# Kernel optimization log

Measured on AMD Instinct MI355X. Metric: run time of the kernel, lower is better.

## Reference

```python
import jax, jax.numpy as jnp
import numpy as np

B, S, D_ENC, D_DEC, UNITS = 32, 2048, 1024, 1024, 1024


def setup_inputs() -> dict:
    key = jax.random.key(0)
    k1, k2, k3, k4 = jax.random.split(key, 4)
    h_encoder = jax.random.normal(k1, (B, S, D_ENC), dtype=jnp.float32)
    h_decoder_prev = jax.random.normal(k2, (B, D_DEC), dtype=jnp.float32)
    # Dense1: (D_ENC + D_DEC) -> UNITS, tanh; Dense2: UNITS -> 1, relu
    W1 = jax.random.normal(k3, (D_ENC + D_DEC, UNITS), dtype=jnp.float32) * 0.02
    b1 = jnp.zeros((UNITS,), dtype=jnp.float32)
    W2 = jax.random.normal(k4, (UNITS, 1), dtype=jnp.float32) * 0.02
    b2 = jnp.zeros((1,), dtype=jnp.float32)
    return {"h_encoder": h_encoder, "h_decoder_prev": h_decoder_prev,
            "W1": W1, "b1": b1, "W2": W2, "b2": b2}


def reference(h_encoder, h_decoder_prev, W1, b1, W2, b2):
    # Equivalent to concat([h_encoder, repeat(h_decoder)], -1) @ W1 without
    # materializing the repeated/concatenated tensor: split W1 by input block.
    d_enc = h_encoder.shape[-1]
    W1_enc, W1_dec = W1[:d_enc], W1[d_enc:]
    dec_proj = h_decoder_prev @ W1_dec  # [B, UNITS]
    energies1 = jnp.tanh(jnp.einsum('bse,eu->bsu', h_encoder, W1_enc)
                         + dec_proj[:, None, :] + b1)  # [B, S, UNITS]
    energies2 = jax.nn.relu(jnp.einsum('bsu,uo->bso', energies1, W2) + b2)  # [B, S, 1]
    attention_weights = jax.nn.softmax(energies2, axis=1)  # softmax over seq axis
    # repeat along last dim + multiply + reduce_sum == broadcast-weighted sum
    context_vector = jnp.sum(attention_weights * h_encoder, axis=1)  # [B, D_ENC]
    return (context_vector, attention_weights)
```

## Files before the change

kernel.cpp:

```cpp
#include <hip/hip_runtime.h>
#include <cstdint>
#include <cstddef>

#define BB 32
#define SS 2048
#define DD 1024
#define MM (BB * SS)

typedef __bf16 bf16_t;
typedef __bf16 bf16x4 __attribute__((ext_vector_type(4)));
typedef __bf16 bf16x8 __attribute__((ext_vector_type(8)));
typedef float  f32x4  __attribute__((ext_vector_type(4)));

typedef __attribute__((address_space(1))) unsigned int gu32;
typedef __attribute__((address_space(3))) unsigned int lu32;

__device__ __forceinline__ void async_copy16(const void* g, void* l) {
  __builtin_amdgcn_global_load_lds((gu32*)g, (lu32*)l, 16, 0, 0);
}

__global__ __launch_bounds__(256) void convert_henc_kernel(
    const float* __restrict__ h, bf16_t* __restrict__ o) {
  const size_t base = ((size_t)blockIdx.x * 256 + threadIdx.x) * 8;
#pragma unroll
  for (int it = 0; it < 16; ++it) {
    const size_t off = base + (size_t)it * 4194304;
    const float4 a = *(const float4*)(h + off);
    const float4 b = *(const float4*)(h + off + 4);
    bf16x8 r;
    r[0] = (bf16_t)a.x; r[1] = (bf16_t)a.y; r[2] = (bf16_t)a.z; r[3] = (bf16_t)a.w;
    r[4] = (bf16_t)b.x; r[5] = (bf16_t)b.y; r[6] = (bf16_t)b.z; r[7] = (bf16_t)b.w;
    *(bf16x8*)(o + off) = r;
  }
}

__global__ __launch_bounds__(256) void conv_w1t_kernel(
    const float* __restrict__ W1, bf16_t* __restrict__ W1T) {
  __shared__ float tile[64][65];
  const int bk = (blockIdx.x & 15) * 64;
  const int bn = (blockIdx.x >> 4) * 64;
  const int tx = threadIdx.x & 63;
  const int ty = threadIdx.x >> 6;
#pragma unroll
  for (int i = 0; i < 16; ++i) {
    const int kr = i * 4 + ty;
    tile[kr][tx] = W1[(size_t)(bk + kr) * 1024 + bn + tx];
  }
  __syncthreads();
#pragma unroll
  for (int i = 0; i < 16; ++i) {
    const int nr = i * 4 + ty;
    W1T[(size_t)(bn + nr) * 1024 + bk + tx] = (bf16_t)tile[tx][nr];
  }
}

__global__ __launch_bounds__(256) void dec_proj_kernel(
    const float* __restrict__ hDec, const float* __restrict__ W1,
    const float* __restrict__ b1, float* __restrict__ dp,
    float* __restrict__ e2) {
  __shared__ float sred[256];
  const int bidx = blockIdx.x;
  const int b  = bidx >> 3;
  const int uc = bidx & 7;
  const int t  = threadIdx.x;
  if (e2) e2[bidx * 256 + t] = 0.f;
  const int u  = uc * 128 + (t & 127);
  const int kh = t >> 7;
  const float* wd = W1 + (size_t)1024 * 1024 + u;
  const float* hd = hDec + b * 1024 + kh * 512;
  float acc = 0.f;
#pragma unroll 4
  for (int k = 0; k < 512; ++k)
    acc += hd[k] * wd[(size_t)(kh * 512 + k) * 1024];
  sred[t] = acc;
  __syncthreads();
  if (t < 128) dp[b * 1024 + u] = sred[t] + sred[t + 128] + b1[u];
}

__global__ __launch_bounds__(256, 3) void fused_gemm_v2(
    const bf16_t* __restrict__ hEncB, const bf16_t* __restrict__ W1T,
    const float* __restrict__ dp, const float* __restrict__ W2,
    float* __restrict__ e2p) {
  __shared__ bf16_t sA[2 * 128 * 32];
  __shared__ bf16_t sB[2 * 128 * 32];

  const int tid  = threadIdx.x;
  const int lane = tid & 63;
  const int wv   = tid >> 6;
  const int wm   = wv >> 1;
  const int wn   = wv & 1;

  const int bid   = blockIdx.x;
  const int mtile = ((bid >> 6) << 3) | (bid & 7);
  const int nblk  = (bid >> 3) & 7;
  const int m0    = mtile * 128;
  const int n0    = nblk * 128;
  const int b     = m0 >> 11;

  const int col = lane & 15;
  const int q   = lane >> 4;
  const int sw  = q ^ ((col >> 1) & 3);

  f32x4 acc[4][4];
#pragma unroll
  for (int mi = 0; mi < 4; ++mi)
#pragma unroll
    for (int ni = 0; ni < 4; ++ni)
      acc[mi][ni] = (f32x4){0.f, 0.f, 0.f, 0.f};

  char* sAc = (char*)sA;
  char* sBc = (char*)sB;

  const int lrow = lane >> 2;
  const int lc   = (lane & 3) ^ ((lane >> 3) & 3);
  const int s0   = wv * 2, s1 = wv * 2 + 1;
  const bf16_t* bG0 = W1T   + (size_t)(n0 + s0 * 16 + lrow) * 1024 + lc * 8;
  const bf16_t* bG1 = W1T   + (size_t)(n0 + s1 * 16 + lrow) * 1024 + lc * 8;
  const bf16_t* aG0 = hEncB + (size_t)(m0 + s0 * 16 + lrow) * 1024 + lc * 8;
  const bf16_t* aG1 = hEncB + (size_t)(m0 + s1 * 16 + lrow) * 1024 + lc * 8;

  const unsigned a_rd = (unsigned)((wm * 64 + col) * 64 + sw * 16);
  const unsigned b_rd = (unsigned)((wn * 64 + col) * 64 + sw * 16);

#pragma unroll 1
  for (int k0 = 0; k0 < 1024; k0 += 64) {
    async_copy16(aG0 + k0,      sAc + s0 * 1024);
    async_copy16(aG1 + k0,      sAc + s1 * 1024);
    async_copy16(aG0 + k0 + 32, sAc + 8192 + s0 * 1024);
    async_copy16(aG1 + k0 + 32, sAc + 8192 + s1 * 1024);
    async_copy16(bG0 + k0,      sBc + s0 * 1024);
    async_copy16(bG1 + k0,      sBc + s1 * 1024);
    async_copy16(bG0 + k0 + 32, sBc + 8192 + s0 * 1024);
    async_copy16(bG1 + k0 + 32, sBc + 8192 + s1 * 1024);
    __syncthreads();
#pragma unroll
    for (int pl = 0; pl < 2; ++pl) {
      bf16x8 af[4], bf[4];
#pragma unroll
      for (int mi = 0; mi < 4; ++mi)
        af[mi] = *(const bf16x8*)(sAc + pl * 8192 + a_rd + mi * 1024);
#pragma unroll
      for (int ni = 0; ni < 4; ++ni)
        bf[ni] = *(const bf16x8*)(sBc + pl * 8192 + b_rd + ni * 1024);
#pragma unroll
      for (int mi = 0; mi < 4; ++mi)
#pragma unroll
        for (int ni = 0; ni < 4; ++ni)
          acc[mi][ni] = __builtin_amdgcn_mfma_f32_16x16x32_bf16(af[mi], bf[ni], acc[mi][ni], 0, 0, 0);
    }
    __syncthreads();
  }

  float rs[4][4];
#pragma unroll
  for (int mi = 0; mi < 4; ++mi)
#pragma unroll
    for (int r = 0; r < 4; ++r) rs[mi][r] = 0.f;

  const float* dpb = dp + b * 1024 + n0 + wn * 64 + col;
  const float* w2b = W2 + n0 + wn * 64 + col;
#pragma unroll
  for (int ni = 0; ni < 4; ++ni) {
    const float dpn = dpb[ni * 16];
    const float w2n = w2b[ni * 16];
#pragma unroll
    for (int mi = 0; mi < 4; ++mi)
#pragma unroll
      for (int r = 0; r < 4; ++r) {
        const float x = acc[mi][ni][r] + dpn;
        const float e = __expf(2.f * x);
        const float th = 1.f - 2.f / (e + 1.f);
        rs[mi][r] += th * w2n;
      }
  }
#pragma unroll
  for (int off = 1; off < 16; off <<= 1)
#pragma unroll
    for (int mi = 0; mi < 4; ++mi)
#pragma unroll
      for (int r = 0; r < 4; ++r)
        rs[mi][r] += __shfl_xor(rs[mi][r], off, 64);
  if (col == 0) {
    float* dst = e2p + (size_t)(nblk * 2 + wn) * MM + m0 + wm * 64 + q * 4;
#pragma unroll
    for (int mi = 0; mi < 4; ++mi) {
      f32x4 o4 = {rs[mi][0], rs[mi][1], rs[mi][2], rs[mi][3]};
      *(f32x4*)(dst + mi * 16) = o4;
    }
  }
}

__global__ __launch_bounds__(256) void softmax_v2(
    const float* __restrict__ e2p, const float* __restrict__ b2,
    float* __restrict__ attn) {
  const int b = blockIdx.x;
  const int t = threadIdx.x;
  __shared__ float sred[4];
  const float b2v = b2[0];
  float v[8];
  float lmax = 0.f;
#pragma unroll
  for (int i = 0; i < 8; ++i) {
    const float* p = e2p + b * 2048 + i * 256 + t;
    float s = 0.f;
#pragma unroll
    for (int ps = 0; ps < 16; ++ps) s += p[(size_t)ps * MM];
    v[i] = fmaxf(s + b2v, 0.f);
    lmax = fmaxf(lmax, v[i]);
  }
#pragma unroll
  for (int off = 1; off < 64; off <<= 1) lmax = fmaxf(lmax, __shfl_xor(lmax, off, 64));
  const int wv = t >> 6;
  const int lane = t & 63;
  if (lane == 0) sred[wv] = lmax;
  __syncthreads();
  const float bmax = fmaxf(fmaxf(sred[0], sred[1]), fmaxf(sred[2], sred[3]));
  __syncthreads();
  float ev[8];
  float lsum = 0.f;
#pragma unroll
  for (int i = 0; i < 8; ++i) { ev[i] = __expf(v[i] - bmax); lsum += ev[i]; }
#pragma unroll
  for (int off = 1; off < 64; off <<= 1) lsum += __shfl_xor(lsum, off, 64);
  if (lane == 0) sred[wv] = lsum;
  __syncthreads();
  const float inv = 1.f / (sred[0] + sred[1] + sred[2] + sred[3]);
#pragma unroll
  for (int i = 0; i < 8; ++i) attn[b * 2048 + i * 256 + t] = ev[i] * inv;
}

__global__ __launch_bounds__(256) void context_v2(
    const bf16_t* __restrict__ hEncB, const float* __restrict__ attn,
    float* __restrict__ ctxp) {
  const int b = blockIdx.x >> 3;
  const int c = blockIdx.x & 7;
  const int t = threadIdx.x;
  const int tx = t & 127;
  const int ty = t >> 7;
  __shared__ float w[256];
  w[t] = attn[b * 2048 + c * 256 + t];
  __syncthreads();
  float a[8];
#pragma unroll
  for (int k = 0; k < 8; ++k) a[k] = 0.f;
  const bf16_t* base = hEncB + ((size_t)b * 2048 + c * 256 + ty) * 1024 + tx * 8;
#pragma unroll 4
  for (int j = 0; j < 128; ++j) {
    const bf16x8 h8 = *(const bf16x8*)(base + (size_t)j * 2048);
    const float ws = w[j * 2 + ty];
#pragma unroll
    for (int k = 0; k < 8; ++k) a[k] += ws * (float)h8[k];
  }
  float* o = ctxp + ((size_t)(c * 2 + ty)) * 32768 + b * 1024 + tx * 8;
  f32x4 lo = {a[0], a[1], a[2], a[3]};
  f32x4 hi = {a[4], a[5], a[6], a[7]};
  *(f32x4*)(o)     = lo;
  *(f32x4*)(o + 4) = hi;
}

__global__ __launch_bounds__(256) void ctx_reduce(
    const float* __restrict__ ctxp, float* __restrict__ ctx) {
  const int idx = blockIdx.x * 256 + threadIdx.x;
  f32x4 s = {0.f, 0.f, 0.f, 0.f};
#pragma unroll
  for (int p = 0; p < 16; ++p)
    s += *(const f32x4*)(ctxp + (size_t)p * 32768 + (size_t)idx * 4);
  *(f32x4*)(ctx + (size_t)idx * 4) = s;
}

__global__ __launch_bounds__(256, 3) void fused_gemm_v1(
    const float* __restrict__ hEnc, const bf16_t* __restrict__ W1T,
    const float* __restrict__ dp, const float* __restrict__ W2,
    float* __restrict__ e2) {
  __shared__ bf16_t sA[2 * 128 * 32];
  __shared__ bf16_t sB[2 * 128 * 32];

  const int tid  = threadIdx.x;
  const int lane = tid & 63;
  const int wv   = tid >> 6;
  const int wm   = wv >> 1;
  const int wn   = wv & 1;

  const int bid   = blockIdx.x;
  const int mtile = ((bid >> 6) << 3) | (bid & 7);
  const int nblk  = (bid >> 3) & 7;
  const int m0    = mtile * 128;
  const int n0    = nblk * 128;
  const int b     = m0 >> 11;

  const int col = lane & 15;
  const int q   = lane >> 4;
  const int sw  = q ^ ((col >> 1) & 3);

  f32x4 acc[4][4];
#pragma unroll
  for (int mi = 0; mi < 4; ++mi)
#pragma unroll
    for (int ni = 0; ni < 4; ++ni)
      acc[mi][ni] = (f32x4){0.f, 0.f, 0.f, 0.f};

  char* sAc = (char*)sA;
  char* sBc = (char*)sB;

  const int lrow = lane >> 2;
  const int lc   = (lane & 3) ^ ((lane >> 3) & 3);
  const int s0   = wv * 2, s1 = wv * 2 + 1;
  const bf16_t* bG0 = W1T + (size_t)(n0 + s0 * 16 + lrow) * 1024 + lc * 8;
  const bf16_t* bG1 = W1T + (size_t)(n0 + s1 * 16 + lrow) * 1024 + lc * 8;

  const int frow = tid >> 3;
  const int fc   = tid & 7;
  const float* aG = hEnc + (size_t)(m0 + frow) * 1024 + fc * 4;
  const unsigned f_off =
      frow * 64u + (unsigned)(((fc >> 1) ^ ((frow >> 1) & 3)) << 4) + (unsigned)(fc & 1) * 8u;

  const unsigned a_rd = (unsigned)((wm * 64 + col) * 64 + sw * 16);
  const unsigned b_rd = (unsigned)((wn * 64 + col) * 64 + sw * 16);

#pragma unroll 1
  for (int k0 = 0; k0 < 1024; k0 += 64) {
    async_copy16(bG0 + k0,      sBc + s0 * 1024);
    async_copy16(bG1 + k0,      sBc + s1 * 1024);
    async_copy16(bG0 + k0 + 32, sBc + 8192 + s0 * 1024);
    async_copy16(bG1 + k0 + 32, sBc + 8192 + s1 * 1024);
#pragma unroll
    for (int pl = 0; pl < 2; ++pl)
#pragma unroll
      for (int i = 0; i < 4; ++i) {
        const float4 v = *(const float4*)(aG + k0 + pl * 32 + (size_t)i * 32 * 1024);
        bf16x4 a4;
        a4[0] = (bf16_t)v.x; a4[1] = (bf16_t)v.y;
        a4[2] = (bf16_t)v.z; a4[3] = (bf16_t)v.w;
        *(bf16x4*)(sAc + pl * 8192 + f_off + i * 2048) = a4;
      }
    __syncthreads();
#pragma unroll
    for (int pl = 0; pl < 2; ++pl) {
      bf16x8 af[4], bf[4];
#pragma unroll
      for (int mi = 0; mi < 4; ++mi)
        af[mi] = *(const bf16x8*)(sAc + pl * 8192 + a_rd + mi * 1024);
#pragma unroll
      for (int ni = 0; ni < 4; ++ni)
        bf[ni] = *(const bf16x8*)(sBc + pl * 8192 + b_rd + ni * 1024);
#pragma unroll
      for (int mi = 0; mi < 4; ++mi)
#pragma unroll
        for (int ni = 0; ni < 4; ++ni)
          acc[mi][ni] = __builtin_amdgcn_mfma_f32_16x16x32_bf16(af[mi], bf[ni], acc[mi][ni], 0, 0, 0);
    }
    __syncthreads();
  }

  float rs[4][4];
#pragma unroll
  for (int mi = 0; mi < 4; ++mi)
#pragma unroll
    for (int r = 0; r < 4; ++r) rs[mi][r] = 0.f;

  const float* dpb = dp + b * 1024 + n0 + wn * 64 + col;
  const float* w2b = W2 + n0 + wn * 64 + col;
#pragma unroll
  for (int ni = 0; ni < 4; ++ni) {
    const float dpn = dpb[ni * 16];
    const float w2n = w2b[ni * 16];
#pragma unroll
    for (int mi = 0; mi < 4; ++mi)
#pragma unroll
      for (int r = 0; r < 4; ++r) {
        const float x = acc[mi][ni][r] + dpn;
        const float e = __expf(2.f * x);
        const float th = 1.f - 2.f / (e + 1.f);
        rs[mi][r] += th * w2n;
      }
  }
#pragma unroll
  for (int off = 1; off < 16; off <<= 1)
#pragma unroll
    for (int mi = 0; mi < 4; ++mi)
#pragma unroll
      for (int r = 0; r < 4; ++r)
        rs[mi][r] += __shfl_xor(rs[mi][r], off, 64);
  if (col == 0) {
#pragma unroll
    for (int mi = 0; mi < 4; ++mi)
#pragma unroll
      for (int r = 0; r < 4; ++r)
        atomicAdd(&e2[m0 + wm * 64 + mi * 16 + q * 4 + r], rs[mi][r]);
  }
}

__global__ __launch_bounds__(256) void softmax_v1(
    const float* __restrict__ e2, const float* __restrict__ b2,
    float* __restrict__ attn, float* __restrict__ ctx) {
  const int b = blockIdx.x;
  const int t = threadIdx.x;
  __shared__ float sred[4];
  const float b2v = b2[0];
  float v[8];
  float lmax = 0.f;
#pragma unroll
  for (int i = 0; i < 8; ++i) {
    v[i] = fmaxf(e2[b * 2048 + i * 256 + t] + b2v, 0.f);
    lmax = fmaxf(lmax, v[i]);
  }
#pragma unroll
  for (int off = 1; off < 64; off <<= 1) lmax = fmaxf(lmax, __shfl_xor(lmax, off, 64));
  const int wv = t >> 6;
  const int lane = t & 63;
  if (lane == 0) sred[wv] = lmax;
  __syncthreads();
  const float bmax = fmaxf(fmaxf(sred[0], sred[1]), fmaxf(sred[2], sred[3]));
  __syncthreads();
  float ev[8];
  float lsum = 0.f;
#pragma unroll
  for (int i = 0; i < 8; ++i) { ev[i] = __expf(v[i] - bmax); lsum += ev[i]; }
#pragma unroll
  for (int off = 1; off < 64; off <<= 1) lsum += __shfl_xor(lsum, off, 64);
  if (lane == 0) sred[wv] = lsum;
  __syncthreads();
  const float inv = 1.f / (sred[0] + sred[1] + sred[2] + sred[3]);
#pragma unroll
  for (int i = 0; i < 8; ++i) attn[b * 2048 + i * 256 + t] = ev[i] * inv;
#pragma unroll
  for (int i = 0; i < 4; ++i) ctx[b * 1024 + i * 256 + t] = 0.f;
}

__global__ __launch_bounds__(256) void context_v1(
    const float* __restrict__ hEnc, const float* __restrict__ attn,
    float* __restrict__ ctx) {
  const int b = blockIdx.x >> 3;
  const int c = blockIdx.x & 7;
  const int t = threadIdx.x;
  __shared__ float w[256];
  w[t] = attn[b * 2048 + c * 256 + t];
  __syncthreads();
  float ax = 0.f, ay = 0.f, az = 0.f, aw = 0.f;
  const float* base = hEnc + ((size_t)b * 2048 + c * 256) * 1024 + t * 4;
#pragma unroll 8
  for (int s = 0; s < 256; ++s) {
    const float4 h4 = *(const float4*)(base + (size_t)s * 1024);
    const float ws = w[s];
    ax += ws * h4.x; ay += ws * h4.y; az += ws * h4.z; aw += ws * h4.w;
  }
  float* o = ctx + b * 1024 + t * 4;
  atomicAdd(o + 0, ax);
  atomicAdd(o + 1, ay);
  atomicAdd(o + 2, az);
  atomicAdd(o + 3, aw);
}

extern "C" void kernel_launch(void* const* d_in, const int* in_sizes, int n_in,
                              void* d_out, int out_size, void* d_ws, size_t ws_size,
                              hipStream_t stream) {
  const float* hEnc = (const float*)d_in[0];
  const float* hDec = (const float*)d_in[1];
  const float* W1   = (const float*)d_in[2];
  const float* b1   = (const float*)d_in[3];
  const float* W2   = (const float*)d_in[4];
  const float* b2   = (const float*)d_in[5];
  float* out = (float*)d_out;

  char* ws = (char*)d_ws;

  const size_t OFF_HENC = 0;
  const size_t OFF_W1T  = 134217728;
  const size_t OFF_DP   = OFF_W1T + 2097152;
  const size_t OFF_E2P  = OFF_DP  + 131072;
  const size_t OFF_CTXP = OFF_E2P + 4194304;
  const size_t NEED     = OFF_CTXP + 2097152;

  if (ws_size >= NEED) {
    bf16_t* hEncB = (bf16_t*)(ws + OFF_HENC);
    bf16_t* W1T   = (bf16_t*)(ws + OFF_W1T);
    float*  dp    = (float*)(ws + OFF_DP);
    float*  e2p   = (float*)(ws + OFF_E2P);
    float*  ctxp  = (float*)(ws + OFF_CTXP);

    convert_henc_kernel<<<2048, 256, 0, stream>>>(hEnc, hEncB);
    conv_w1t_kernel<<<256, 256, 0, stream>>>(W1, W1T);
    dec_proj_kernel<<<256, 256, 0, stream>>>(hDec, W1, b1, dp, nullptr);
    fused_gemm_v2<<<4096, 256, 0, stream>>>(hEncB, W1T, dp, W2, e2p);
    softmax_v2<<<32, 256, 0, stream>>>(e2p, b2, out + 32768);
    context_v2<<<256, 256, 0, stream>>>(hEncB, out + 32768, ctxp);
    ctx_reduce<<<32, 256, 0, stream>>>(ctxp, out);
  } else {
    bf16_t* W1T = (bf16_t*)ws;
    float*  dp  = (float*)(ws + 2u * 1024 * 1024);
    float*  e2  = (float*)(ws + 2u * 1024 * 1024 + 128u * 1024);

    conv_w1t_kernel<<<256, 256, 0, stream>>>(W1, W1T);
    dec_proj_kernel<<<256, 256, 0, stream>>>(hDec, W1, b1, dp, e2);
    fused_gemm_v1<<<4096, 256, 0, stream>>>(hEnc, W1T, dp, W2, e2);
    softmax_v1<<<32, 256, 0, stream>>>(e2, b2, out + 32768, out);
    context_v1<<<256, 256, 0, stream>>>(hEnc, out + 32768, out);
  }
}
```

Before: 629.7 us.

## Fuse fp32-to-bf16 conversion of encoder states into the pipelined GEMM

```diff
diff --git a/kernel.cpp b/kernel.cpp
--- a/kernel.cpp
+++ b/kernel.cpp
@@ -17,21 +17,6 @@
 
 __device__ __forceinline__ void async_copy16(const void* g, void* l) {
   __builtin_amdgcn_global_load_lds((gu32*)g, (lu32*)l, 16, 0, 0);
-}
-
-__global__ __launch_bounds__(256) void convert_henc_kernel(
-    const float* __restrict__ h, bf16_t* __restrict__ o) {
-  const size_t base = ((size_t)blockIdx.x * 256 + threadIdx.x) * 8;
-#pragma unroll
-  for (int it = 0; it < 16; ++it) {
-    const size_t off = base + (size_t)it * 4194304;
-    const float4 a = *(const float4*)(h + off);
-    const float4 b = *(const float4*)(h + off + 4);
-    bf16x8 r;
-    r[0] = (bf16_t)a.x; r[1] = (bf16_t)a.y; r[2] = (bf16_t)a.z; r[3] = (bf16_t)a.w;
-    r[4] = (bf16_t)b.x; r[5] = (bf16_t)b.y; r[6] = (bf16_t)b.z; r[7] = (bf16_t)b.w;
-    *(bf16x8*)(o + off) = r;
-  }
 }
 
 __global__ __launch_bounds__(256) void conv_w1t_kernel(
@@ -56,14 +41,12 @@
 
 __global__ __launch_bounds__(256) void dec_proj_kernel(
     const float* __restrict__ hDec, const float* __restrict__ W1,
-    const float* __restrict__ b1, float* __restrict__ dp,
-    float* __restrict__ e2) {
+    const float* __restrict__ b1, float* __restrict__ dp) {
   __shared__ float sred[256];
   const int bidx = blockIdx.x;
   const int b  = bidx >> 3;
   const int uc = bidx & 7;
   const int t  = threadIdx.x;
-  if (e2) e2[bidx * 256 + t] = 0.f;
   const int u  = uc * 128 + (t & 127);
   const int kh = t >> 7;
   const float* wd = W1 + (size_t)1024 * 1024 + u;
@@ -77,12 +60,12 @@
   if (t < 128) dp[b * 1024 + u] = sred[t] + sred[t + 128] + b1[u];
 }
 
-__global__ __launch_bounds__(256, 3) void fused_gemm_v2(
-    const bf16_t* __restrict__ hEncB, const bf16_t* __restrict__ W1T,
+__global__ __launch_bounds__(256, 2) void fused_gemm_v3(
+    const float* __restrict__ hEnc, const bf16_t* __restrict__ W1T,
     const float* __restrict__ dp, const float* __restrict__ W2,
     float* __restrict__ e2p) {
-  __shared__ bf16_t sA[2 * 128 * 32];
-  __shared__ bf16_t sB[2 * 128 * 32];
+  __shared__ bf16_t sA[128 * 64];
+  __shared__ bf16_t sB[2][128 * 64];
 
   const int tid  = threadIdx.x;
   const int lane = tid & 63;
@@ -109,30 +92,63 @@
       acc[mi][ni] = (f32x4){0.f, 0.f, 0.f, 0.f};
 
   char* sAc = (char*)sA;
-  char* sBc = (char*)sB;
+  char* sBc = (char*)&sB[0][0];
 
   const int lrow = lane >> 2;
   const int lc   = (lane & 3) ^ ((lane >> 3) & 3);
   const int s0   = wv * 2, s1 = wv * 2 + 1;
-  const bf16_t* bG0 = W1T   + (size_t)(n0 + s0 * 16 + lrow) * 1024 + lc * 8;
-  const bf16_t* bG1 = W1T   + (size_t)(n0 + s1 * 16 + lrow) * 1024 + lc * 8;
-  const bf16_t* aG0 = hEncB + (size_t)(m0 + s0 * 16 + lrow) * 1024 + lc * 8;
-  const bf16_t* aG1 = hEncB + (size_t)(m0 + s1 * 16 + lrow) * 1024 + lc * 8;
+  const bf16_t* bG0 = W1T + (size_t)(n0 + s0 * 16 + lrow) * 1024 + lc * 8;
+  const bf16_t* bG1 = W1T + (size_t)(n0 + s1 * 16 + lrow) * 1024 + lc * 8;
+
+  const int r0  = tid >> 3;
+  const int oct = tid & 7;
+  const float* aG = hEnc + (size_t)(m0 + r0) * 1024 + oct * 8;
+  const unsigned wOff = (unsigned)(((oct >> 2) * 8192) + r0 * 64 +
+                                   (((oct & 3) ^ ((r0 >> 1) & 3)) << 4));
 
   const unsigned a_rd = (unsigned)((wm * 64 + col) * 64 + sw * 16);
   const unsigned b_rd = (unsigned)((wn * 64 + col) * 64 + sw * 16);
 
+  async_copy16(bG0,      sBc + s0 * 1024);
+  async_copy16(bG1,      sBc + s1 * 1024);
+  async_copy16(bG0 + 32, sBc + 8192 + s0 * 1024);
+  async_copy16(bG1 + 32, sBc + 8192 + s1 * 1024);
+  float4 ar[4][2];
+#pragma unroll
+  for (int i = 0; i < 4; ++i) {
+    ar[i][0] = *(const float4*)(aG + (size_t)i * 32 * 1024);
+    ar[i][1] = *(const float4*)(aG + (size_t)i * 32 * 1024 + 4);
+  }
+
+  int c = 0;
 #pragma unroll 1
-  for (int k0 = 0; k0 < 1024; k0 += 64) {
-    async_copy16(aG0 + k0,      sAc + s0 * 1024);
-    async_copy16(aG1 + k0,      sAc + s1 * 1024);
-    async_copy16(aG0 + k0 + 32, sAc + 8192 + s0 * 1024);
-    async_copy16(aG1 + k0 + 32, sAc + 8192 + s1 * 1024);
-    async_copy16(bG0 + k0,      sBc + s0 * 1024);
-    async_copy16(bG1 + k0,      sBc + s1 * 1024);
-    async_copy16(bG0 + k0 + 32, sBc + 8192 + s0 * 1024);
-    async_copy16(bG1 + k0 + 32, sBc + 8192 + s1 * 1024);
+  for (int t = 0; t < 16; ++t) {
+#pragma unroll
+    for (int i = 0; i < 4; ++i) {
+      bf16x8 a8;
+      a8[0] = (bf16_t)ar[i][0].x; a8[1] = (bf16_t)ar[i][0].y;
+      a8[2] = (bf16_t)ar[i][0].z; a8[3] = (bf16_t)ar[i][0].w;
+      a8[4] = (bf16_t)ar[i][1].x; a8[5] = (bf16_t)ar[i][1].y;
+      a8[6] = (bf16_t)ar[i][1].z; a8[7] = (bf16_t)ar[i][1].w;
+      *(bf16x8*)(sAc + wOff + i * 2048) = a8;
+    }
     __syncthreads();
+
+    if (t < 15) {
+      const int kn = t * 64 + 64;
+      char* nb = sBc + (c ^ 1) * 16384;
+      async_copy16(bG0 + kn,      nb + s0 * 1024);
+      async_copy16(bG1 + kn,      nb + s1 * 1024);
+      async_copy16(bG0 + kn + 32, nb + 8192 + s0 * 1024);
+      async_copy16(bG1 + kn + 32, nb + 8192 + s1 * 1024);
+#pragma unroll
+      for (int i = 0; i < 4; ++i) {
+        ar[i][0] = *(const float4*)(aG + kn + (size_t)i * 32 * 1024);
+        ar[i][1] = *(const float4*)(aG + kn + (size_t)i * 32 * 1024 + 4);
+      }
+    }
+
+    const char* sBr = sBc + c * 16384;
 #pragma unroll
     for (int pl = 0; pl < 2; ++pl) {
       bf16x8 af[4], bf[4];
@@ -141,14 +157,16 @@
         af[mi] = *(const bf16x8*)(sAc + pl * 8192 + a_rd + mi * 1024);
 #pragma unroll
       for (int ni = 0; ni < 4; ++ni)
-        bf[ni] = *(const bf16x8*)(sBc + pl * 8192 + b_rd + ni * 1024);
+        bf[ni] = *(const bf16x8*)(sBr + pl * 8192 + b_rd + ni * 1024);
 #pragma unroll
       for (int mi = 0; mi < 4; ++mi)
 #pragma unroll
         for (int ni = 0; ni < 4; ++ni)
           acc[mi][ni] = __builtin_amdgcn_mfma_f32_16x16x32_bf16(af[mi], bf[ni], acc[mi][ni], 0, 0, 0);
     }
-    __syncthreads();
+    __builtin_amdgcn_s_barrier();
+    __builtin_amdgcn_sched_barrier(0);
+    c ^= 1;
   }
 
   float rs[4][4];
@@ -229,226 +247,35 @@
   for (int i = 0; i < 8; ++i) attn[b * 2048 + i * 256 + t] = ev[i] * inv;
 }
 
-__global__ __launch_bounds__(256) void context_v2(
-    const bf16_t* __restrict__ hEncB, const float* __restrict__ attn,
+__global__ __launch_bounds__(256) void context_v3(
+    const float* __restrict__ hEnc, const float* __restrict__ attn,
     float* __restrict__ ctxp) {
   const int b = blockIdx.x >> 3;
-  const int c = blockIdx.x & 7;
-  const int t = threadIdx.x;
-  const int tx = t & 127;
-  const int ty = t >> 7;
-  __shared__ float w[256];
-  w[t] = attn[b * 2048 + c * 256 + t];
-  __syncthreads();
-  float a[8];
-#pragma unroll
-  for (int k = 0; k < 8; ++k) a[k] = 0.f;
-  const bf16_t* base = hEncB + ((size_t)b * 2048 + c * 256 + ty) * 1024 + tx * 8;
-#pragma unroll 4
-  for (int j = 0; j < 128; ++j) {
-    const bf16x8 h8 = *(const bf16x8*)(base + (size_t)j * 2048);
-    const float ws = w[j * 2 + ty];
-#pragma unroll
-    for (int k = 0; k < 8; ++k) a[k] += ws * (float)h8[k];
-  }
-  float* o = ctxp + ((size_t)(c * 2 + ty)) * 32768 + b * 1024 + tx * 8;
-  f32x4 lo = {a[0], a[1], a[2], a[3]};
-  f32x4 hi = {a[4], a[5], a[6], a[7]};
-  *(f32x4*)(o)     = lo;
-  *(f32x4*)(o + 4) = hi;
-}
-
-__global__ __launch_bounds__(256) void ctx_reduce(
-    const float* __restrict__ ctxp, float* __restrict__ ctx) {
-  const int idx = blockIdx.x * 256 + threadIdx.x;
-  f32x4 s = {0.f, 0.f, 0.f, 0.f};
-#pragma unroll
-  for (int p = 0; p < 16; ++p)
-    s += *(const f32x4*)(ctxp + (size_t)p * 32768 + (size_t)idx * 4);
-  *(f32x4*)(ctx + (size_t)idx * 4) = s;
-}
-
-__global__ __launch_bounds__(256, 3) void fused_gemm_v1(
-    const float* __restrict__ hEnc, const bf16_t* __restrict__ W1T,
-    const float* __restrict__ dp, const float* __restrict__ W2,
-    float* __restrict__ e2) {
-  __shared__ bf16_t sA[2 * 128 * 32];
-  __shared__ bf16_t sB[2 * 128 * 32];
-
-  const int tid  = threadIdx.x;
-  const int lane = tid & 63;
-  const int wv   = tid >> 6;
-  const int wm   = wv >> 1;
-  const int wn   = wv & 1;
-
-  const int bid   = blockIdx.x;
-  const int mtile = ((bid >> 6) << 3) | (bid & 7);
-  const int nblk  = (bid >> 3) & 7;
-  const int m0    = mtile * 128;
-  const int n0    = nblk * 128;
-  const int b     = m0 >> 11;
-
-  const int col = lane & 15;
-  const int q   = lane >> 4;
-  const int sw  = q ^ ((col >> 1) & 3);
-
-  f32x4 acc[4][4];
-#pragma unroll
-  for (int mi = 0; mi < 4; ++mi)
-#pragma unroll
-    for (int ni = 0; ni < 4; ++ni)
-      acc[mi][ni] = (f32x4){0.f, 0.f, 0.f, 0.f};
-
-  char* sAc = (char*)sA;
-  char* sBc = (char*)sB;
-
-  const int lrow = lane >> 2;
-  const int lc   = (lane & 3) ^ ((lane >> 3) & 3);
-  const int s0   = wv * 2, s1 = wv * 2 + 1;
-  const bf16_t* bG0 = W1T + (size_t)(n0 + s0 * 16 + lrow) * 1024 + lc * 8;
-  const bf16_t* bG1 = W1T + (size_t)(n0 + s1 * 16 + lrow) * 1024 + lc * 8;
-
-  const int frow = tid >> 3;
-  const int fc   = tid & 7;
-  const float* aG = hEnc + (size_t)(m0 + frow) * 1024 + fc * 4;
-  const unsigned f_off =
-      frow * 64u + (unsigned)(((fc >> 1) ^ ((frow >> 1) & 3)) << 4) + (unsigned)(fc & 1) * 8u;
-
-  const unsigned a_rd = (unsigned)((wm * 64 + col) * 64 + sw * 16);
-  const unsigned b_rd = (unsigned)((wn * 64 + col) * 64 + sw * 16);
-
-#pragma unroll 1
-  for (int k0 = 0; k0 < 1024; k0 += 64) {
-    async_copy16(bG0 + k0,      sBc + s0 * 1024);
-    async_copy16(bG1 + k0,      sBc + s1 * 1024);
-    async_copy16(bG0 + k0 + 32, sBc + 8192 + s0 * 1024);
-    async_copy16(bG1 + k0 + 32, sBc + 8192 + s1 * 1024);
-#pragma unroll
-    for (int pl = 0; pl < 2; ++pl)
-#pragma unroll
-      for (int i = 0; i < 4; ++i) {
-        const float4 v = *(const float4*)(aG + k0 + pl * 32 + (size_t)i * 32 * 1024);
-        bf16x4 a4;
-        a4[0] = (bf16_t)v.x; a4[1] = (bf16_t)v.y;
-        a4[2] = (bf16_t)v.z; a4[3] = (bf16_t)v.w;
-        *(bf16x4*)(sAc + pl * 8192 + f_off + i * 2048) = a4;
-      }
-    __syncthreads();
-#pragma unroll
-    for (int pl = 0; pl < 2; ++pl) {
-      bf16x8 af[4], bf[4];
-#pragma unroll
-      for (int mi = 0; mi < 4; ++mi)
-        af[mi] = *(const bf16x8*)(sAc + pl * 8192 + a_rd + mi * 1024);
-#pragma unroll
-      for (int ni = 0; ni < 4; ++ni)
-        bf[ni] = *(const bf16x8*)(sBc + pl * 8192 + b_rd + ni * 1024);
-#pragma unroll
-      for (int mi = 0; mi < 4; ++mi)
-#pragma unroll
-        for (int ni = 0; ni < 4; ++ni)
-          acc[mi][ni] = __builtin_amdgcn_mfma_f32_16x16x32_bf16(af[mi], bf[ni], acc[mi][ni], 0, 0, 0);
-    }
-    __syncthreads();
-  }
-
-  float rs[4][4];
-#pragma unroll
-  for (int mi = 0; mi < 4; ++mi)
-#pragma unroll
-    for (int r = 0; r < 4; ++r) rs[mi][r] = 0.f;
-
-  const float* dpb = dp + b * 1024 + n0 + wn * 64 + col;
-  const float* w2b = W2 + n0 + wn * 64 + col;
-#pragma unroll
-  for (int ni = 0; ni < 4; ++ni) {
-    const float dpn = dpb[ni * 16];
-    const float w2n = w2b[ni * 16];
-#pragma unroll
-    for (int mi = 0; mi < 4; ++mi)
-#pragma unroll
-      for (int r = 0; r < 4; ++r) {
-        const float x = acc[mi][ni][r] + dpn;
-        const float e = __expf(2.f * x);
-        const float th = 1.f - 2.f / (e + 1.f);
-        rs[mi][r] += th * w2n;
-      }
-  }
-#pragma unroll
-  for (int off = 1; off < 16; off <<= 1)
-#pragma unroll
-    for (int mi = 0; mi < 4; ++mi)
-#pragma unroll
-      for (int r = 0; r < 4; ++r)
-        rs[mi][r] += __shfl_xor(rs[mi][r], off, 64);
-  if (col == 0) {
-#pragma unroll
-    for (int mi = 0; mi < 4; ++mi)
-#pragma unroll
-      for (int r = 0; r < 4; ++r)
-        atomicAdd(&e2[m0 + wm * 64 + mi * 16 + q * 4 + r], rs[mi][r]);
-  }
-}
-
-__global__ __launch_bounds__(256) void softmax_v1(
-    const float* __restrict__ e2, const float* __restrict__ b2,
-    float* __restrict__ attn, float* __restrict__ ctx) {
-  const int b = blockIdx.x;
-  const int t = threadIdx.x;
-  __shared__ float sred[4];
-  const float b2v = b2[0];
-  float v[8];
-  float lmax = 0.f;
-#pragma unroll
-  for (int i = 0; i < 8; ++i) {
-    v[i] = fmaxf(e2[b * 2048 + i * 256 + t] + b2v, 0.f);
-    lmax = fmaxf(lmax, v[i]);
-  }
-#pragma unroll
-  for (int off = 1; off < 64; off <<= 1) lmax = fmaxf(lmax, __shfl_xor(lmax, off, 64));
-  const int wv = t >> 6;
-  const int lane = t & 63;
-  if (lane == 0) sred[wv] = lmax;
-  __syncthreads();
-  const float bmax = fmaxf(fmaxf(sred[0], sred[1]), fmaxf(sred[2], sred[3]));
-  __syncthreads();
-  float ev[8];
-  float lsum = 0.f;
-#pragma unroll
-  for (int i = 0; i < 8; ++i) { ev[i] = __expf(v[i] - bmax); lsum += ev[i]; }
-#pragma unroll
-  for (int off = 1; off < 64; off <<= 1) lsum += __shfl_xor(lsum, off, 64);
-  if (lane == 0) sred[wv] = lsum;
-  __syncthreads();
-  const float inv = 1.f / (sred[0] + sred[1] + sred[2] + sred[3]);
-#pragma unroll
-  for (int i = 0; i < 8; ++i) attn[b * 2048 + i * 256 + t] = ev[i] * inv;
-#pragma unroll
-  for (int i = 0; i < 4; ++i) ctx[b * 1024 + i * 256 + t] = 0.f;
-}
-
-__global__ __launch_bounds__(256) void context_v1(
-    const float* __restrict__ hEnc, const float* __restrict__ attn,
-    float* __restrict__ ctx) {
-  const int b = blockIdx.x >> 3;
-  const int c = blockIdx.x & 7;
+  const int cks = blockIdx.x & 7;
   const int t = threadIdx.x;
   __shared__ float w[256];
-  w[t] = attn[b * 2048 + c * 256 + t];
+  w[t] = attn[b * 2048 + cks * 256 + t];
   __syncthreads();
   float ax = 0.f, ay = 0.f, az = 0.f, aw = 0.f;
-  const float* base = hEnc + ((size_t)b * 2048 + c * 256) * 1024 + t * 4;
+  const float* base = hEnc + ((size_t)b * 2048 + cks * 256) * 1024 + t * 4;
 #pragma unroll 8
   for (int s = 0; s < 256; ++s) {
     const float4 h4 = *(const float4*)(base + (size_t)s * 1024);
     const float ws = w[s];
     ax += ws * h4.x; ay += ws * h4.y; az += ws * h4.z; aw += ws * h4.w;
   }
-  float* o = ctx + b * 1024 + t * 4;
-  atomicAdd(o + 0, ax);
-  atomicAdd(o + 1, ay);
-  atomicAdd(o + 2, az);
-  atomicAdd(o + 3, aw);
+  f32x4 o4 = {ax, ay, az, aw};
+  *(f32x4*)(ctxp + (size_t)cks * 32768 + b * 1024 + t * 4) = o4;
+}
+
+__global__ __launch_bounds__(256) void ctx_reduce8(
+    const float* __restrict__ ctxp, float* __restrict__ ctx) {
+  const int idx = blockIdx.x * 256 + threadIdx.x;
+  f32x4 s = {0.f, 0.f, 0.f, 0.f};
+#pragma unroll
+  for (int p = 0; p < 8; ++p)
+    s += *(const f32x4*)(ctxp + (size_t)p * 32768 + (size_t)idx * 4);
+  *(f32x4*)(ctx + (size_t)idx * 4) = s;
 }
 
 extern "C" void kernel_launch(void* const* d_in, const int* in_sizes, int n_in,
@@ -463,37 +290,15 @@
   float* out = (float*)d_out;
 
   char* ws = (char*)d_ws;
-
-  const size_t OFF_HENC = 0;
-  const size_t OFF_W1T  = 134217728;
-  const size_t OFF_DP   = OFF_W1T + 2097152;
-  const size_t OFF_E2P  = OFF_DP  + 131072;
-  const size_t OFF_CTXP = OFF_E2P + 4194304;
-  const size_t NEED     = OFF_CTXP + 2097152;
-
-  if (ws_size >= NEED) {
-    bf16_t* hEncB = (bf16_t*)(ws + OFF_HENC);
-    bf16_t* W1T   = (bf16_t*)(ws + OFF_W1T);
-    float*  dp    = (float*)(ws + OFF_DP);
-    float*  e2p   = (float*)(ws + OFF_E2P);
-    float*  ctxp  = (float*)(ws + OFF_CTXP);
-
-    convert_henc_kernel<<<2048, 256, 0, stream>>>(hEnc, hEncB);
-    conv_w1t_kernel<<<256, 256, 0, stream>>>(W1, W1T);
-    dec_proj_kernel<<<256, 256, 0, stream>>>(hDec, W1, b1, dp, nullptr);
-    fused_gemm_v2<<<4096, 256, 0, stream>>>(hEncB, W1T, dp, W2, e2p);
-    softmax_v2<<<32, 256, 0, stream>>>(e2p, b2, out + 32768);
-    context_v2<<<256, 256, 0, stream>>>(hEncB, out + 32768, ctxp);
-    ctx_reduce<<<32, 256, 0, stream>>>(ctxp, out);
-  } else {
-    bf16_t* W1T = (bf16_t*)ws;
-    float*  dp  = (float*)(ws + 2u * 1024 * 1024);
-    float*  e2  = (float*)(ws + 2u * 1024 * 1024 + 128u * 1024);
-
-    conv_w1t_kernel<<<256, 256, 0, stream>>>(W1, W1T);
-    dec_proj_kernel<<<256, 256, 0, stream>>>(hDec, W1, b1, dp, e2);
-    fused_gemm_v1<<<4096, 256, 0, stream>>>(hEnc, W1T, dp, W2, e2);
-    softmax_v1<<<32, 256, 0, stream>>>(e2, b2, out + 32768, out);
-    context_v1<<<256, 256, 0, stream>>>(hEnc, out + 32768, out);
-  }
-}
+  bf16_t* W1T  = (bf16_t*)ws;
+  float*  dp   = (float*)(ws + 2u * 1024 * 1024);
+  float*  e2p  = (float*)(ws + 2u * 1024 * 1024 + 128u * 1024);
+  float*  ctxp = (float*)(ws + 6u * 1024 * 1024 + 128u * 1024);
+
+  conv_w1t_kernel<<<256, 256, 0, stream>>>(W1, W1T);
+  dec_proj_kernel<<<256, 256, 0, stream>>>(hDec, W1, b1, dp);
+  fused_gemm_v3<<<4096, 256, 0, stream>>>(hEnc, W1T, dp, W2, e2p);
+  softmax_v2<<<32, 256, 0, stream>>>(e2p, b2, out + 32768);
+  context_v3<<<256, 256, 0, stream>>>(hEnc, out + 32768, ctxp);
+  ctx_reduce8<<<32, 256, 0, stream>>>(ctxp, out);
+}
```

After: 614.1 us. 1.03x faster.
